# Kernel tuning notes

Measured on AMD Instinct MI355X. Metric: run time of the kernel, lower is better.

The kernel has to match this reference:

```python
import jax, jax.numpy as jnp
from jax import lax
import numpy as np

THRESHOLD = 0.9
KHALF = 5  # conv_kernel_size; full conv width = 2*KHALF + 1 = 11


def _cif_scan(eouts, alpha_norm, elens, ylens, Lp1):
    """Vectorized-over-batch integrate-and-fire scan over time (lax.scan)."""
    B, T, D = eouts.shape
    bidx = jnp.arange(B)
    dt = eouts.dtype

    def step(carry, xs):
        alpha_accum, state, n_tok, fired = carry
        a_t, e_t, t = xs  # a_t: [B], e_t: [B,D], t: scalar int
        alpha_accum = alpha_accum + a_t
        active = (t <= elens - 1) & (n_tok < ylens)
        fire = active & (alpha_accum >= THRESHOLD)
        ak1 = 1.0 - alpha_accum
        ak2 = a_t - ak1
        # attention-weight column for time t
        aw_col = jnp.zeros((B, Lp1), dt)
        w_old = jnp.where(fire, ak1, jnp.where(active, a_t, jnp.zeros((), dt)))
        aw_col = aw_col.at[bidx, n_tok].add(w_old)
        n_new = n_tok + fire.astype(n_tok.dtype)
        aw_col = aw_col.at[bidx, n_new].add(jnp.where(fire, ak2, jnp.zeros((), dt)))
        # fired output row (set once per token slot)
        fire_val = state + ak1[:, None] * e_t
        cur = fired[bidx, n_tok]
        fired = fired.at[bidx, n_tok].set(jnp.where(fire[:, None], fire_val, cur))
        # integrate / reset state
        state = jnp.where(fire[:, None], ak2[:, None] * e_t,
                          jnp.where(active[:, None], state + a_t[:, None] * e_t, state))
        alpha_accum = jnp.where(fire, ak2, alpha_accum)
        return (alpha_accum, state, n_new, fired), aw_col

    init = (jnp.zeros((B,), dt), jnp.zeros((B, D), dt),
            jnp.zeros((B,), jnp.int32), jnp.zeros((B, Lp1, D), dt))
    xs = (jnp.swapaxes(alpha_norm, 0, 1), jnp.swapaxes(eouts, 0, 1),
          jnp.arange(T))
    (_, _, _, fired), aw_cols = lax.scan(step, init, xs)
    aws = jnp.transpose(aw_cols, (1, 2, 0))[:, None]  # [B,1,Lp1,T]
    return fired, aws


def _forward(eouts, conv_w, conv_b, proj_w, proj_b, elens, ylens, L):
    # Conv1d over time, 'same' padding: [B,T,D] -> [B,T,C]
    conv_feat = lax.conv_general_dilated(
        eouts, conv_w, window_strides=(1,), padding=[(KHALF, KHALF)],
        dimension_numbers=('NWC', 'WIO', 'NWC')) + conv_b
    alpha = jax.nn.sigmoid(conv_feat @ proj_w + proj_b)[:, :, 0]  # [B,T]
    alpha_norm = alpha / jnp.sum(alpha, axis=1, keepdims=True) \
        * ylens[:, None].astype(alpha.dtype)
    fired, aws = _cif_scan(eouts, alpha_norm, elens, ylens, L + 1)
    return fired[:, :L], alpha, aws


def setup_inputs():
    key = jax.random.key(0)
    k1, k2, k3, k4, k5 = jax.random.split(key, 5)
    B, T, D, C = 16, 2048, 512, 512
    eouts = jax.random.normal(k1, (B, T, D), jnp.float32)
    elens = jnp.maximum(jax.random.randint(k2, (B,), 0, T), T // 2).astype(jnp.int32)
    ylens = jnp.maximum(jax.random.randint(k3, (B,), 0, 128), 32).astype(jnp.int32)
    conv_w = jax.random.normal(k4, (2 * KHALF + 1, D, C), jnp.float32) * 0.02
    conv_b = jnp.zeros((C,), jnp.float32)
    proj_w = jax.random.normal(k5, (C, 1), jnp.float32) * 0.05
    proj_b = jnp.zeros((1,), jnp.float32)
    return dict(eouts=eouts, conv_w=conv_w, conv_b=conv_b,
                proj_w=proj_w, proj_b=proj_b, elens=elens, ylens=ylens)


def reference(eouts, conv_w, conv_b, proj_w, proj_b, elens, ylens):
    L = int(jnp.max(ylens))  # max_len = ylens.max(), as in the original
    return _forward(eouts, conv_w, conv_b, proj_w, proj_b, elens, ylens, L)
```

## Files before the change

kernel.cpp:

```cpp
#include <hip/hip_runtime.h>
#include <math.h>

#define KHALF 5
#define MAXF 256

__global__ void k_weff(const float* __restrict__ conv_w, const float* __restrict__ conv_b,
                       const float* __restrict__ proj_w, const float* __restrict__ proj_b,
                       float* __restrict__ w_eff, float* __restrict__ b_eff,
                       int KD, int C) {
    int gid = blockIdx.x * blockDim.x + threadIdx.x;
    int wave = gid >> 6;
    int lane = gid & 63;
    if (wave > KD) return;
    float s = 0.f;
    if (wave < KD) {
        const float* row = conv_w + (size_t)wave * C;
        for (int c = lane * 4; c < C; c += 256) {
            float4 v = *reinterpret_cast<const float4*>(row + c);
            float4 w = *reinterpret_cast<const float4*>(proj_w + c);
            s += v.x * w.x + v.y * w.y + v.z * w.z + v.w * w.w;
        }
    } else {
        for (int c = lane; c < C; c += 64) s += conv_b[c] * proj_w[c];
    }
#pragma unroll
    for (int off = 32; off > 0; off >>= 1) s += __shfl_down(s, off, 64);
    if (lane == 0) {
        if (wave < KD) w_eff[wave] = s;
        else           b_eff[0] = s + proj_b[0];
    }
}

__global__ __launch_bounds__(256) void k_qdot(const float* __restrict__ eouts,
                                              const float* __restrict__ w_eff,
                                              float* __restrict__ q, int BT) {
    __shared__ float tile[64 * 68];
    __shared__ float wls[11 * 68];
    __shared__ float part[64 * 49];
    const int u0 = blockIdx.x * 64;
    const int lane = threadIdx.x & 63;
    const int sw = threadIdx.x >> 6;
    float acc[11];
#pragma unroll
    for (int k = 0; k < 11; ++k) acc[k] = 0.f;
    for (int c = 0; c < 8; ++c) {
        __syncthreads();
#pragma unroll
        for (int it = 0; it < 4; ++it) {
            int idx = it * 256 + threadIdx.x;
            int r = idx >> 4, j4 = idx & 15;
            float4 v = *reinterpret_cast<const float4*>(
                eouts + (size_t)(u0 + r) * 512 + c * 64 + j4 * 4);
            *reinterpret_cast<float4*>(&tile[r * 68 + j4 * 4]) = v;
        }
        if (threadIdx.x < 176) {
            int k = threadIdx.x >> 4, sl = threadIdx.x & 15;
            float4 wv = *reinterpret_cast<const float4*>(
                w_eff + k * 512 + c * 64 + sl * 4);
            *reinterpret_cast<float4*>(&wls[k * 68 + sl * 4]) = wv;
        }
        __syncthreads();
#pragma unroll
        for (int j4 = 0; j4 < 4; ++j4) {
            float4 av = *reinterpret_cast<const float4*>(&tile[lane * 68 + sw * 16 + j4 * 4]);
            int dl = sw * 16 + j4 * 4;
#pragma unroll
            for (int k = 0; k < 11; ++k) {
                float4 wv = *reinterpret_cast<const float4*>(&wls[k * 68 + dl]);
                acc[k] += av.x * wv.x + av.y * wv.y + av.z * wv.z + av.w * wv.w;
            }
        }
    }
    __syncthreads();
#pragma unroll
    for (int k = 0; k < 11; ++k) part[lane * 49 + sw * 12 + k] = acc[k];
    __syncthreads();
    if (threadIdx.x < 64) {
        int r = threadIdx.x;
        const float* p = &part[r * 49];
        float o[12];
#pragma unroll
        for (int k = 0; k < 11; ++k)
            o[k] = (p[k] + p[12 + k]) + (p[24 + k] + p[36 + k]);
        o[11] = 0.f;
        float4* dst = reinterpret_cast<float4*>(q + (size_t)(u0 + r) * 12);
        dst[0] = make_float4(o[0], o[1], o[2], o[3]);
        dst[1] = make_float4(o[4], o[5], o[6], o[7]);
        dst[2] = make_float4(o[8], o[9], o[10], o[11]);
    }
}

__global__ __launch_bounds__(256) void k_sigpart(const float* __restrict__ q,
                                                 const float* __restrict__ b_eff,
                                                 float* __restrict__ alpha,
                                                 float* __restrict__ partials,
                                                 int T, int tcb) {
    __shared__ float qs[266 * 12];
    __shared__ float psm[4];
    int bx = blockIdx.x;
    int b = bx / tcb, tc = bx % tcb;
    int t0 = tc * 256;
    const float* qb = q + (size_t)b * T * 12;
    const int base = (t0 - 5) * 12;
    const int lim = T * 12;
    for (int i = threadIdx.x; i < 266 * 12; i += 256) {
        int gi = base + i;
        qs[i] = (gi >= 0 && gi < lim) ? qb[gi] : 0.f;
    }
    __syncthreads();
    int t = t0 + threadIdx.x;
    float sacc = b_eff[0];
#pragma unroll
    for (int k = 0; k < 11; ++k) sacc += qs[(threadIdx.x + k) * 12 + k];
    float al = 1.f / (1.f + expf(-sacc));
    alpha[(size_t)b * T + t] = al;
    float s = al;
    int lane = threadIdx.x & 63;
    int w = threadIdx.x >> 6;
#pragma unroll
    for (int off = 32; off > 0; off >>= 1) s += __shfl_down(s, off, 64);
    if (lane == 0) psm[w] = s;
    __syncthreads();
    if (threadIdx.x == 0) {
        float tot = 0.f;
        for (int i = 0; i < 4; ++i) tot += psm[i];
        partials[bx] = tot;
    }
}

__global__ void k_alpha(const float* __restrict__ eouts,
                        const float* __restrict__ w_eff,
                        const float* __restrict__ b_eff,
                        float* __restrict__ alpha,
                        int B, int T, int D) {
    const int W = 2 * KHALF + 1;
    int gid = blockIdx.x * blockDim.x + threadIdx.x;
    int wave = gid >> 6;
    int lane = gid & 63;
    if (wave >= B * T) return;
    int b = wave / T;
    int t = wave - b * T;
    int WD = W * D;
    int t0 = t - KHALF;
    float s = 0.f;
    if (t0 >= 0 && t0 + W <= T) {
        const float* base = eouts + ((size_t)b * T + t0) * D;
        for (int j = lane * 4; j < WD; j += 256) {
            float4 v = *reinterpret_cast<const float4*>(base + j);
            float4 w = *reinterpret_cast<const float4*>(w_eff + j);
            s += v.x * w.x + v.y * w.y + v.z * w.z + v.w * w.w;
        }
    } else {
        const float* base = eouts + (size_t)b * T * D;
        for (int j = lane; j < WD; j += 64) {
            int tt = t0 + j / D;
            if (tt >= 0 && tt < T) {
                int d = j - (j / D) * D;
                s += base[(size_t)tt * D + d] * w_eff[j];
            }
        }
    }
#pragma unroll
    for (int off = 32; off > 0; off >>= 1) s += __shfl_down(s, off, 64);
    if (lane == 0) {
        float logit = s + b_eff[0];
        alpha[(size_t)b * T + t] = 1.f / (1.f + expf(-logit));
    }
}

__global__ void k_chain(const float* __restrict__ alpha_in,
                        int use_part,
                        const float* __restrict__ partials, int npart,
                        const int* __restrict__ elens,
                        const int* __restrict__ ylens,
                        float* __restrict__ alpha_sum,
                        int* __restrict__ n_fired,
                        int* __restrict__ fire_t,
                        float* __restrict__ fire_a1,
                        float* __restrict__ fire_a2,
                        int T, int Lp1) {
    extern __shared__ float an[];
    __shared__ float sm[16];
    __shared__ float stot;
    int b = blockIdx.x;
    const float* row = alpha_in + (size_t)b * T;
    for (int i = threadIdx.x; i < T; i += blockDim.x) an[i] = row[i];
    __syncthreads();
    if (use_part) {
        if (threadIdx.x == 0) {
            float tot = 0.f;
            for (int i = 0; i < npart; ++i) tot += partials[b * npart + i];
            stot = tot;
            alpha_sum[b] = tot;
        }
    } else {
        float s = 0.f;
        for (int i = threadIdx.x; i < T; i += blockDim.x) s += an[i];
        int lane0 = threadIdx.x & 63;
        int w0 = threadIdx.x >> 6;
#pragma unroll
        for (int off = 32; off > 0; off >>= 1) s += __shfl_down(s, off, 64);
        if (lane0 == 0) sm[w0] = s;
        __syncthreads();
        if (threadIdx.x == 0) {
            float tot = 0.f;
            int nw = blockDim.x >> 6;
            for (int i = 0; i < nw; ++i) tot += sm[i];
            stot = tot;
            alpha_sum[b] = tot;
        }
    }
    __syncthreads();
    float ssum = stot;
    float yl = (float)ylens[b];
    for (int i = threadIdx.x; i < T; i += blockDim.x) an[i] = an[i] / ssum * yl;
    __syncthreads();
    if (threadIdx.x >= 64) return;
    int lane = threadIdx.x;
    int elen = elens[b];
    if (elen > T) elen = T;
    const int ylen = ylens[b];
    int* __restrict__ ft = fire_t + (size_t)b * Lp1;
    float* __restrict__ fa1 = fire_a1 + (size_t)b * Lp1;
    float* __restrict__ fa2 = fire_a2 + (size_t)b * Lp1;
    float accum = 0.f;
    int n = 0;
    bool done = false;
    for (int t0 = 0; t0 < elen && !done; t0 += 64) {
        int nv = elen - t0;
        if (nv > 64) nv = 64;
        float a = (lane < nv) ? an[t0 + lane] : 0.f;
        float P = a;
#pragma unroll
        for (int off = 1; off < 64; off <<= 1) {
            float tmp = __shfl_up(P, off, 64);
            if (lane >= off) P += tmp;
        }
        unsigned long long validmask = (nv == 64) ? ~0ull : ((1ull << nv) - 1ull);
        float base = accum;
        int start = 0;
        while (true) {
            bool cond = (base + P >= 0.9f);
            unsigned long long bal = __ballot(cond) & validmask;
            if (start > 0) bal &= (~0ull) << start;
            if (bal == 0) break;
            int u = __builtin_ctzll(bal);
            float Pu = __shfl(P, u, 64);
            float au = __shfl(a, u, 64);
            float accum_f = base + Pu;
            float ak1 = 1.f - accum_f;
            float ak2 = au - ak1;
            if (lane == 0) { ft[n] = t0 + u; fa1[n] = ak1; fa2[n] = ak2; }
            ++n;
            if (n >= ylen) { done = true; break; }
            base = ak2 - Pu;
            start = u + 1;
            if (start >= nv) break;
        }
        if (!done) {
            float Plast = __shfl(P, nv - 1, 64);
            accum = base + Plast;
        }
    }
    if (lane == 0) n_fired[b] = n;
}

__global__ void k_awfired(const float* __restrict__ eouts,
                          const float* __restrict__ alpha,
                          const float* __restrict__ alpha_sum,
                          const int* __restrict__ elens,
                          const int* __restrict__ ylens,
                          const int* __restrict__ n_fired,
                          const int* __restrict__ fire_t,
                          const float* __restrict__ fire_a1,
                          const float* __restrict__ fire_a2,
                          float* __restrict__ aws,
                          float* __restrict__ fired,
                          int T, int D, int L, int Lp1,
                          int AB, int tcpb, int DB) {
    if ((int)blockIdx.x < AB) {
        __shared__ int fts[MAXF];
        __shared__ float a1s[MAXF];
        __shared__ float a2s[MAXF];
        int b = blockIdx.x / tcpb;
        int tc = blockIdx.x % tcpb;
        int nf = n_fired[b];
        for (int i = threadIdx.x; i < nf; i += blockDim.x) {
            fts[i] = fire_t[(size_t)b * Lp1 + i];
            a1s[i] = fire_a1[(size_t)b * Lp1 + i];
            a2s[i] = fire_a2[(size_t)b * Lp1 + i];
        }
        __syncthreads();
        int t = tc * 256 + threadIdx.x;
        if (t >= T) return;
        int elen = elens[b];
        if (elen > T) elen = T;
        int ylen = ylens[b];
        bool active = (t < elen);
        int rowi = 0;
        bool isfire = false;
        float v1 = 0.f, v2 = 0.f;
        if (active) {
            int lo = 0, hi = nf;
            while (lo < hi) {
                int mid = (lo + hi) >> 1;
                if (fts[mid] < t) lo = mid + 1; else hi = mid;
            }
            rowi = lo;
            isfire = (rowi < nf && fts[rowi] == t);
            if (isfire) { v1 = a1s[rowi]; v2 = a2s[rowi]; }
            else if (rowi < ylen) v1 = alpha[(size_t)b * T + t] / alpha_sum[b] * (float)ylen;
            else active = false;
        }
        float* col = aws + (size_t)b * Lp1 * T + t;
        for (int r = 0; r < Lp1; ++r) {
            float v = 0.f;
            if (active) {
                if (r == rowi) v = v1;
                else if (isfire && r == rowi + 1) v = v2;
            }
            col[(size_t)r * T] = v;
        }
    } else {
        int idx = blockIdx.x - AB;
        int b = idx / (L * DB);
        int rem = idx % (L * DB);
        int n = rem / DB;
        int d = (rem % DB) * 256 + threadIdx.x;
        if (d >= D) return;
        int nf = n_fired[b];
        float* dst = fired + ((size_t)b * L + n) * D + d;
        if (n >= nf) { *dst = 0.f; return; }
        int t0 = (n == 0) ? 0 : fire_t[(size_t)b * Lp1 + n - 1];
        int t1 = fire_t[(size_t)b * Lp1 + n];
        float ak1 = fire_a1[(size_t)b * Lp1 + n];
        float ak2p = (n > 0) ? fire_a2[(size_t)b * Lp1 + n - 1] : 0.f;
        float ssum = alpha_sum[b];
        float yl = (float)ylens[b];
        const float* e = eouts + ((size_t)b * T + t0) * D + d;
        float accv = 0.f;
        for (int t = t0; t <= t1; ++t, e += D) {
            float wgt;
            if (t == t1) wgt = ak1;
            else if (t == t0 && n > 0) wgt = ak2p;
            else wgt = alpha[(size_t)b * T + t] / ssum * yl;
            accv += wgt * e[0];
        }
        *dst = accv;
    }
}

extern "C" void kernel_launch(void* const* d_in, const int* in_sizes, int n_in,
                              void* d_out, int out_size, void* d_ws, size_t ws_size,
                              hipStream_t stream) {
    const float* eouts  = (const float*)d_in[0];
    const float* conv_w = (const float*)d_in[1];
    const float* conv_b = (const float*)d_in[2];
    const float* proj_w = (const float*)d_in[3];
    const float* proj_b = (const float*)d_in[4];
    const int*   elens  = (const int*)d_in[5];
    const int*   ylens  = (const int*)d_in[6];

    const int B = in_sizes[5];
    const int C = in_sizes[2];
    const int W = 2 * KHALF + 1;
    const int D = in_sizes[1] / (W * C);
    const int T = in_sizes[0] / (B * D);
    const int L = (out_size - 2 * B * T) / (B * (D + T));
    const int Lp1 = L + 1;
    const int BT = B * T;
    const int tcb = (T + 255) / 256;

    float* out   = (float*)d_out;
    float* fired = out;
    float* alpha = out + (size_t)B * L * D;
    float* aws   = alpha + (size_t)B * T;

    char*  ws        = (char*)d_ws;
    float* w_eff     = (float*)ws;
    float* b_eff     = (float*)(ws + (size_t)W * D * 4);
    float* alpha_sum = b_eff + 16;
    int*   n_fired   = (int*)(alpha_sum + B + 16);
    int*   fire_t    = n_fired + B + 16;
    float* fire_a1   = (float*)(fire_t + (size_t)B * Lp1 + 16);
    float* fire_a2   = fire_a1 + (size_t)B * Lp1 + 16;
    float* qbuf      = fire_a2 + (size_t)B * Lp1 + 16;
    float* partials  = qbuf + (size_t)BT * 12 + 16;
    size_t ws_need   = (size_t)((char*)(partials + (size_t)B * tcb + 16) - ws);

    const int KD = W * D;
    {
        long long threads = (long long)(KD + 1) * 64;
        int blocks = (int)((threads + 255) / 256);
        k_weff<<<blocks, 256, 0, stream>>>(conv_w, conv_b, proj_w, proj_b,
                                           w_eff, b_eff, KD, C);
    }

    const bool fast = (ws_size >= ws_need) && (D == 512) && (C == 512) &&
                      (BT % 64 == 0) && (T % 256 == 0) && (T <= 16384) &&
                      (Lp1 <= MAXF);
    if (fast) {
        k_qdot<<<BT / 64, 256, 0, stream>>>(eouts, w_eff, qbuf, BT);
        k_sigpart<<<B * tcb, 256, 0, stream>>>(qbuf, b_eff, alpha, partials, T, tcb);
    } else {
        long long threads = (long long)BT * 64;
        int blocks = (int)((threads + 255) / 256);
        k_alpha<<<blocks, 256, 0, stream>>>(eouts, w_eff, b_eff, alpha, B, T, D);
    }

    k_chain<<<B, 256, T * sizeof(float), stream>>>(
        alpha, fast ? 1 : 0, partials, tcb,
        elens, ylens, alpha_sum,
        n_fired, fire_t, fire_a1, fire_a2, T, Lp1);

    {
        int tcpb = (T + 255) / 256;
        int AB = B * tcpb;
        int DB = (D + 255) / 256;
        int FB = B * L * DB;
        k_awfired<<<AB + FB, 256, 0, stream>>>(eouts, alpha, alpha_sum,
                                               elens, ylens, n_fired,
                                               fire_t, fire_a1, fire_a2,
                                               aws, fired, T, D, L, Lp1,
                                               AB, tcpb, DB);
    }
}
```

Before: 186.2 us.

## Register-block two rows per thread in qdot and precompute normalized alpha

In k_qdot, the work split changes so each thread handles two rows (rp and rp+32) across eight 8-wide column slices instead of one row across four 16-wide slices. Each weight float4 loaded from LDS is then reused for two rows, cutting LDS traffic per FMA, at the cost of more accumulator registers and a wider partial-sum reduction. Separately, k_chain now writes the normalized alpha to a workspace buffer. k_awfired reads that buffer instead of recomputing alpha/sum*ylen with a division per element.

```diff
diff --git a/kernel.cpp b/kernel.cpp
--- a/kernel.cpp
+++ b/kernel.cpp
@@ -36,13 +36,13 @@
                                               float* __restrict__ q, int BT) {
     __shared__ float tile[64 * 68];
     __shared__ float wls[11 * 68];
-    __shared__ float part[64 * 49];
+    __shared__ float part[64 * 89];
     const int u0 = blockIdx.x * 64;
-    const int lane = threadIdx.x & 63;
-    const int sw = threadIdx.x >> 6;
-    float acc[11];
-#pragma unroll
-    for (int k = 0; k < 11; ++k) acc[k] = 0.f;
+    const int rp = threadIdx.x & 31;
+    const int s8 = threadIdx.x >> 5;
+    float acc0[11], acc1[11];
+#pragma unroll
+    for (int k = 0; k < 11; ++k) { acc0[k] = 0.f; acc1[k] = 0.f; }
     for (int c = 0; c < 8; ++c) {
         __syncthreads();
 #pragma unroll
@@ -61,27 +61,35 @@
         }
         __syncthreads();
 #pragma unroll
-        for (int j4 = 0; j4 < 4; ++j4) {
-            float4 av = *reinterpret_cast<const float4*>(&tile[lane * 68 + sw * 16 + j4 * 4]);
-            int dl = sw * 16 + j4 * 4;
+        for (int j4 = 0; j4 < 2; ++j4) {
+            const int dl = s8 * 8 + j4 * 4;
+            float4 a0 = *reinterpret_cast<const float4*>(&tile[rp * 68 + dl]);
+            float4 a1 = *reinterpret_cast<const float4*>(&tile[(rp + 32) * 68 + dl]);
 #pragma unroll
             for (int k = 0; k < 11; ++k) {
                 float4 wv = *reinterpret_cast<const float4*>(&wls[k * 68 + dl]);
-                acc[k] += av.x * wv.x + av.y * wv.y + av.z * wv.z + av.w * wv.w;
+                acc0[k] += a0.x * wv.x + a0.y * wv.y + a0.z * wv.z + a0.w * wv.w;
+                acc1[k] += a1.x * wv.x + a1.y * wv.y + a1.z * wv.z + a1.w * wv.w;
             }
         }
     }
     __syncthreads();
 #pragma unroll
-    for (int k = 0; k < 11; ++k) part[lane * 49 + sw * 12 + k] = acc[k];
+    for (int k = 0; k < 11; ++k) {
+        part[rp * 89 + s8 * 11 + k] = acc0[k];
+        part[(rp + 32) * 89 + s8 * 11 + k] = acc1[k];
+    }
     __syncthreads();
     if (threadIdx.x < 64) {
         int r = threadIdx.x;
-        const float* p = &part[r * 49];
+        const float* p = &part[r * 89];
         float o[12];
 #pragma unroll
-        for (int k = 0; k < 11; ++k)
-            o[k] = (p[k] + p[12 + k]) + (p[24 + k] + p[36 + k]);
+        for (int k = 0; k < 11; ++k) {
+            float s0 = (p[0 * 11 + k] + p[1 * 11 + k]) + (p[2 * 11 + k] + p[3 * 11 + k]);
+            float s1 = (p[4 * 11 + k] + p[5 * 11 + k]) + (p[6 * 11 + k] + p[7 * 11 + k]);
+            o[k] = s0 + s1;
+        }
         o[11] = 0.f;
         float4* dst = reinterpret_cast<float4*>(q + (size_t)(u0 + r) * 12);
         dst[0] = make_float4(o[0], o[1], o[2], o[3]);
@@ -174,6 +182,7 @@
                         const int* __restrict__ elens,
                         const int* __restrict__ ylens,
                         float* __restrict__ alpha_sum,
+                        float* __restrict__ anorm,
                         int* __restrict__ n_fired,
                         int* __restrict__ fire_t,
                         float* __restrict__ fire_a1,
@@ -213,7 +222,12 @@
     __syncthreads();
     float ssum = stot;
     float yl = (float)ylens[b];
-    for (int i = threadIdx.x; i < T; i += blockDim.x) an[i] = an[i] / ssum * yl;
+    float* __restrict__ anb = anorm + (size_t)b * T;
+    for (int i = threadIdx.x; i < T; i += blockDim.x) {
+        float v = an[i] / ssum * yl;
+        an[i] = v;
+        anb[i] = v;
+    }
     __syncthreads();
     if (threadIdx.x >= 64) return;
     int lane = threadIdx.x;
@@ -266,8 +280,7 @@
 }
 
 __global__ void k_awfired(const float* __restrict__ eouts,
-                          const float* __restrict__ alpha,
-                          const float* __restrict__ alpha_sum,
+                          const float* __restrict__ anorm,
                           const int* __restrict__ elens,
                           const int* __restrict__ ylens,
                           const int* __restrict__ n_fired,
@@ -309,7 +322,7 @@
             rowi = lo;
             isfire = (rowi < nf && fts[rowi] == t);
             if (isfire) { v1 = a1s[rowi]; v2 = a2s[rowi]; }
-            else if (rowi < ylen) v1 = alpha[(size_t)b * T + t] / alpha_sum[b] * (float)ylen;
+            else if (rowi < ylen) v1 = anorm[(size_t)b * T + t];
             else active = false;
         }
         float* col = aws + (size_t)b * Lp1 * T + t;
@@ -335,15 +348,14 @@
         int t1 = fire_t[(size_t)b * Lp1 + n];
         float ak1 = fire_a1[(size_t)b * Lp1 + n];
         float ak2p = (n > 0) ? fire_a2[(size_t)b * Lp1 + n - 1] : 0.f;
-        float ssum = alpha_sum[b];
-        float yl = (float)ylens[b];
+        const float* an_g = anorm + (size_t)b * T;
         const float* e = eouts + ((size_t)b * T + t0) * D + d;
         float accv = 0.f;
         for (int t = t0; t <= t1; ++t, e += D) {
             float wgt;
             if (t == t1) wgt = ak1;
             else if (t == t0 && n > 0) wgt = ak2p;
-            else wgt = alpha[(size_t)b * T + t] / ssum * yl;
+            else wgt = an_g[t];
             accv += wgt * e[0];
         }
         *dst = accv;
@@ -384,7 +396,8 @@
     int*   fire_t    = n_fired + B + 16;
     float* fire_a1   = (float*)(fire_t + (size_t)B * Lp1 + 16);
     float* fire_a2   = fire_a1 + (size_t)B * Lp1 + 16;
-    float* qbuf      = fire_a2 + (size_t)B * Lp1 + 16;
+    float* anorm     = fire_a2 + (size_t)B * Lp1 + 16;
+    float* qbuf      = anorm + (size_t)B * T + 16;
     float* partials  = qbuf + (size_t)BT * 12 + 16;
     size_t ws_need   = (size_t)((char*)(partials + (size_t)B * tcb + 16) - ws);
 
@@ -410,7 +423,7 @@
 
     k_chain<<<B, 256, T * sizeof(float), stream>>>(
         alpha, fast ? 1 : 0, partials, tcb,
-        elens, ylens, alpha_sum,
+        elens, ylens, alpha_sum, anorm,
         n_fired, fire_t, fire_a1, fire_a2, T, Lp1);
 
     {
@@ -418,7 +431,7 @@
         int AB = B * tcpb;
         int DB = (D + 255) / 256;
         int FB = B * L * DB;
-        k_awfired<<<AB + FB, 256, 0, stream>>>(eouts, alpha, alpha_sum,
+        k_awfired<<<AB + FB, 256, 0, stream>>>(eouts, anorm,
                                                elens, ylens, n_fired,
                                                fire_t, fire_a1, fire_a2,
                                                aws, fired, T, D, L, Lp1,
```

Result: faster. 181.7 us (-2.4%).
